# Kernel tuning notes

Hardware: AMD Instinct MI355X
Metric: run time of the kernel (lower is better)

## Reference

```python
import jax, jax.numpy as jnp
import numpy as np

B, S, D = 2, 2048, 768
C = 8                # num_channels
R = D // C           # ternary_rank = 96 (RoPE head_dim)
THETA = 10000.0
TERNARY_STD = 0.2
TERNARY_SCALE = 1.0  # ternary_factor_scaling


def _rope_tables():
    # HF-style RoPE: inv_freq over half dim, emb = concat(freqs, freqs)
    inv_freq = 1.0 / (THETA ** (np.arange(0, R, 2, dtype=np.float32) / R))
    pos = np.arange(S, dtype=np.float32)
    freqs = pos[:, None] * inv_freq[None, :]          # [S, R/2]
    emb = np.concatenate([freqs, freqs], axis=-1)     # [S, R]
    cos = np.broadcast_to(np.cos(emb)[None], (B, S, R)).copy()
    sin = np.broadcast_to(np.sin(emb)[None], (B, S, R)).copy()
    return jnp.asarray(cos), jnp.asarray(sin)


def setup_inputs() -> dict:
    key = jax.random.key(0)
    k1, k2, k3 = jax.random.split(key, 3)
    qz = jax.random.normal(k1, (B, S, D), dtype=jnp.float32)
    U = jax.random.normal(k2, (D, D), dtype=jnp.float32) * TERNARY_STD
    V = jax.random.normal(k3, (D, D), dtype=jnp.float32) * TERNARY_STD
    cos, sin = _rope_tables()
    return {"qz": qz, "cos": cos, "sin": sin, "U": U, "V": V}


def _rotate_half(x):
    h = x.shape[-1] // 2
    return jnp.concatenate([-x[..., h:], x[..., :h]], axis=-1)


def reference(qz, cos, sin, U, V):
    # cos/sin: [B,S,R] -> broadcast over channel dim -> [B,1,S,R]
    cosb = cos[:, None, :, :]
    sinb = sin[:, None, :, :]
    rope = lambda x: x * cosb + _rotate_half(x) * sinb       # apply
    rope_o = lambda x: x * cosb - _rotate_half(x) * sinb     # apply_o (inverse)

    # projections: F.linear(qz, W) == qz @ W.T
    qz_u = (qz @ U.T * TERNARY_SCALE).reshape(B, S, C, R).transpose(0, 2, 1, 3)
    qz_v = (qz @ V.T * TERNARY_SCALE).reshape(B, S, C, R).transpose(0, 2, 1, 3)

    qz_uo = rope_o(qz_u)
    qz_ur = rope(qz_u)
    qz_vr = rope(qz_v)

    # message_F: [B,C,S,S]
    message_F = jnp.einsum('bcqr,bckr->bcqk', qz_ur, qz_vr)
    # softmax(message_F / regularize_h) with regularize_h = 1/D  ->  * D
    qh = jax.nn.softmax((message_F * jnp.float32(D)).astype(jnp.float32), axis=-1).astype(qz_ur.dtype)

    qh_v1 = rope_o(jnp.einsum('bcqk,bckr->bcqr', qh, qz_vr))  # qh @ qz_v
    qh_v2 = rope(jnp.einsum('bckq,bckr->bcqr', qh, qz_uo))    # qh^T @ qz_uo

    qh_v1 = qh_v1.transpose(0, 2, 1, 3).reshape(B, S, D)
    qh_v2 = qh_v2.transpose(0, 2, 1, 3).reshape(B, S, D)

    message_G = (qh_v1 @ U + qh_v2 @ V) * TERNARY_SCALE
    return message_G
```

## Files before the change

### kernel.cpp

```cpp
#include <hip/hip_runtime.h>

typedef _Float16 f16;
typedef _Float16 f16x8 __attribute__((ext_vector_type(8)));
typedef _Float16 f16x4 __attribute__((ext_vector_type(4)));
typedef float f32x4 __attribute__((ext_vector_type(4)));

#define MFMA16(A,B,C) __builtin_amdgcn_mfma_f32_16x16x32_f16(A,B,C,0,0,0)
#define INV2048 4.8828125e-4f
#define HN (16ll*2048*96)
#define UVN 589824
#define ZC1 1107.98979f
#define ZC2 0.54101064f

__device__ __forceinline__ void split_f16(float x, f16& h, f16& l) {
    h = (f16)x;
    l = (f16)((x - (float)h) * 2048.0f);
}

__global__ __launch_bounds__(256) void k0_split(const float* __restrict__ qz,
                                                const float* __restrict__ U,
                                                const float* __restrict__ V,
                                                f16* __restrict__ qzh, f16* __restrict__ qzl,
                                                f16* __restrict__ Uh, f16* __restrict__ Ul,
                                                f16* __restrict__ Vh, f16* __restrict__ Vl) {
    const int i4 = blockIdx.x * 256 + threadIdx.x;
    {
        float4 x = *(const float4*)(qz + (size_t)i4 * 4);
        f16 h0, l0, h1, l1, h2, l2, h3, l3;
        split_f16(x.x, h0, l0); split_f16(x.y, h1, l1);
        split_f16(x.z, h2, l2); split_f16(x.w, h3, l3);
        f16x4 hv = {h0, h1, h2, h3};
        f16x4 lv = {l0, l1, l2, l3};
        *(f16x4*)(qzh + (size_t)i4 * 4) = hv;
        *(f16x4*)(qzl + (size_t)i4 * 4) = lv;
    }
    if (i4 < UVN / 4) {
        float4 x = *(const float4*)(U + (size_t)i4 * 4);
        f16 h0, l0, h1, l1, h2, l2, h3, l3;
        split_f16(x.x, h0, l0); split_f16(x.y, h1, l1);
        split_f16(x.z, h2, l2); split_f16(x.w, h3, l3);
        f16x4 hv = {h0, h1, h2, h3};
        f16x4 lv = {l0, l1, l2, l3};
        *(f16x4*)(Uh + (size_t)i4 * 4) = hv;
        *(f16x4*)(Ul + (size_t)i4 * 4) = lv;
        float4 y = *(const float4*)(V + (size_t)i4 * 4);
        split_f16(y.x, h0, l0); split_f16(y.y, h1, l1);
        split_f16(y.z, h2, l2); split_f16(y.w, h3, l3);
        f16x4 hv2 = {h0, h1, h2, h3};
        f16x4 lv2 = {l0, l1, l2, l3};
        *(f16x4*)(Vh + (size_t)i4 * 4) = hv2;
        *(f16x4*)(Vl + (size_t)i4 * 4) = lv2;
    }
}

__global__ __launch_bounds__(256, 2) void k1_proj(const f16* __restrict__ qzh,
                                                  const f16* __restrict__ qzl,
                                                  const f16* __restrict__ Uh,
                                                  const f16* __restrict__ Ul,
                                                  const f16* __restrict__ Vh,
                                                  const f16* __restrict__ Vl,
                                                  const float* __restrict__ cosb,
                                                  const float* __restrict__ sinb,
                                                  f16* __restrict__ uhp, f16* __restrict__ ulp,
                                                  f16* __restrict__ vhp, f16* __restrict__ vlp,
                                                  f16* __restrict__ vT, f16* __restrict__ oT) {
    __shared__ __align__(16) f16 smem[36864];
    f16* sAh  = smem;
    f16* sAl  = smem + 4608;
    f16* sBuh = smem + 9216;
    f16* sBul = smem + 9216 + 6912;
    f16* sBvh = smem + 9216 + 2 * 6912;
    f16* sBvl = smem + 9216 + 3 * 6912;

    const int tid = threadIdx.x;
    const int w = tid >> 6, lane = tid & 63;
    const int quad = lane >> 4, l15 = lane & 15;
    const int wr = w >> 1, wc = w & 1;
    const int bs0 = blockIdx.x * 64;
    const int c = blockIdx.y;

    const f16* Ug_h = Uh + (size_t)c * 96 * 768;
    const f16* Ug_l = Ul + (size_t)c * 96 * 768;
    const f16* Vg_h = Vh + (size_t)c * 96 * 768;
    const f16* Vg_l = Vl + (size_t)c * 96 * 768;

    f32x4 aUS[2][3] = {}, aUX[2][3] = {};
    f32x4 aVS[2][3] = {}, aVX[2][3] = {};

    for (int k0 = 0; k0 < 768; k0 += 64) {
        __syncthreads();
#pragma unroll
        for (int m = 0; m < 2; ++m) {
            int f = tid + 256 * m, row = f >> 3, cg = f & 7;
            const size_t go = (size_t)(bs0 + row) * 768 + k0 + cg * 8;
            const int lo = row * 72 + cg * 8;
            *(float4*)&sAh[lo] = *(const float4*)(qzh + go);
            *(float4*)&sAl[lo] = *(const float4*)(qzl + go);
        }
#pragma unroll
        for (int m = 0; m < 3; ++m) {
            int f = tid + 256 * m, row = f >> 3, cg = f & 7;
            const size_t go = (size_t)row * 768 + k0 + cg * 8;
            const int lo = row * 72 + cg * 8;
            *(float4*)&sBuh[lo] = *(const float4*)(Ug_h + go);
            *(float4*)&sBul[lo] = *(const float4*)(Ug_l + go);
            *(float4*)&sBvh[lo] = *(const float4*)(Vg_h + go);
            *(float4*)&sBvl[lo] = *(const float4*)(Vg_l + go);
        }
        __syncthreads();
#pragma unroll
        for (int cc = 0; cc < 2; ++cc) {
            f16x8 ah[2], al[2];
#pragma unroll
            for (int mt = 0; mt < 2; ++mt) {
                const int ar = (32 * wr + 16 * mt + l15) * 72 + cc * 32 + quad * 8;
                ah[mt] = *(const f16x8*)&sAh[ar];
                al[mt] = *(const f16x8*)&sAl[ar];
            }
#pragma unroll
            for (int nt = 0; nt < 3; ++nt) {
                const int br = (48 * wc + 16 * nt + l15) * 72 + cc * 32 + quad * 8;
                f16x8 buh = *(const f16x8*)&sBuh[br];
                f16x8 bul = *(const f16x8*)&sBul[br];
                f16x8 bvh = *(const f16x8*)&sBvh[br];
                f16x8 bvl = *(const f16x8*)&sBvl[br];
#pragma unroll
                for (int mt = 0; mt < 2; ++mt) {
                    aUS[mt][nt] = MFMA16(ah[mt], buh, aUS[mt][nt]);
                    aUX[mt][nt] = MFMA16(ah[mt], bul, aUX[mt][nt]);
                    aUX[mt][nt] = MFMA16(al[mt], buh, aUX[mt][nt]);
                    aVS[mt][nt] = MFMA16(ah[mt], bvh, aVS[mt][nt]);
                    aVX[mt][nt] = MFMA16(ah[mt], bvl, aVX[mt][nt]);
                    aVX[mt][nt] = MFMA16(al[mt], bvh, aVX[mt][nt]);
                }
            }
        }
    }

    __syncthreads();
    float* LU = (float*)smem;
    float* LV = LU + 6400;
#pragma unroll
    for (int mt = 0; mt < 2; ++mt)
#pragma unroll
        for (int nt = 0; nt < 3; ++nt)
#pragma unroll
            for (int r = 0; r < 4; ++r) {
                const int sl = 32 * wr + 16 * mt + 4 * quad + r;
                const int col = 48 * wc + 16 * nt + l15;
                LU[sl * 100 + col] = aUS[mt][nt][r] + aUX[mt][nt][r] * INV2048;
                LV[sl * 100 + col] = aVS[mt][nt][r] + aVX[mt][nt][r] * INV2048;
            }
    __syncthreads();

    const int b = bs0 >> 11;
    const int s0 = bs0 & 2047;
    const int head = b * 8 + c;
    const size_t nb = (size_t)head * 2048 * 96;
    const size_t tb = (size_t)head * 96 * 2048;
    const int ty = tid >> 4, tx = tid & 15;

#pragma unroll
    for (int jj = 0; jj < 3; ++jj) {
        int r = tx + 16 * jj;
        f16 vt1[4], vt2[4], ot1[4], ot2[4];
#pragma unroll
        for (int ii = 0; ii < 4; ++ii) {
            int sl = 4 * ty + ii;
            int s = s0 + sl;
            int cbi = (b * 2048 + s) * 96 + r;
            float cc = cosb[cbi], ss = sinb[cbi];
            size_t rowb = nb + (size_t)s * 96;
            float u1 = LU[sl * 100 + r], u2 = LU[sl * 100 + r + 48];
            float v1 = LV[sl * 100 + r], v2 = LV[sl * 100 + r + 48];
            float ur1 = u1 * cc - u2 * ss, ur2 = u2 * cc + u1 * ss;
            float uo1 = u1 * cc + u2 * ss, uo2 = u2 * cc - u1 * ss;
            float vr1 = v1 * cc - v2 * ss, vr2 = v2 * cc + v1 * ss;
            f16 h, l;
            split_f16(ur1, h, l); uhp[rowb + r] = h;      ulp[rowb + r] = l;
            split_f16(ur2, h, l); uhp[rowb + r + 48] = h; ulp[rowb + r + 48] = l;
            split_f16(vr1, h, l); vhp[rowb + r] = h;      vlp[rowb + r] = l;      vt1[ii] = h;
            split_f16(vr2, h, l); vhp[rowb + r + 48] = h; vlp[rowb + r + 48] = l; vt2[ii] = h;
            ot1[ii] = (f16)uo1; ot2[ii] = (f16)uo2;
        }
        f16x4 pv1 = {vt1[0], vt1[1], vt1[2], vt1[3]};
        f16x4 pv2 = {vt2[0], vt2[1], vt2[2], vt2[3]};
        f16x4 po1 = {ot1[0], ot1[1], ot1[2], ot1[3]};
        f16x4 po2 = {ot2[0], ot2[1], ot2[2], ot2[3]};
        *(f16x4*)&vT[tb + (size_t)r * 2048 + s0 + 4 * ty] = pv1;
        *(f16x4*)&vT[tb + (size_t)(r + 48) * 2048 + s0 + 4 * ty] = pv2;
        *(f16x4*)&oT[tb + (size_t)r * 2048 + s0 + 4 * ty] = po1;
        *(f16x4*)&oT[tb + (size_t)(r + 48) * 2048 + s0 + 4 * ty] = po2;
    }
}

__global__ __launch_bounds__(256, 2) void k2_stats(const f16* __restrict__ uhp,
                                                   const f16* __restrict__ ulp,
                                                   const f16* __restrict__ vhp,
                                                   const f16* __restrict__ vlp,
                                                   float* __restrict__ Mo,
                                                   float* __restrict__ Lo) {
    __shared__ f16 Bh[64 * 104];
    __shared__ f16 Bl[64 * 104];
    __shared__ float Mbuf[4][64], Lbuf[4][64];
    const int tid = threadIdx.x, w = tid >> 6, lane = tid & 63;
    const int quad = lane >> 4, l15 = lane & 15;
    const int q0 = blockIdx.x * 64, head = blockIdx.y;
    const f16* Ah_g = uhp + (size_t)head * 2048 * 96;
    const f16* Al_g = ulp + (size_t)head * 2048 * 96;
    const f16* Bh_g = vhp + (size_t)head * 2048 * 96;
    const f16* Bl_g = vlp + (size_t)head * 2048 * 96;

    f16x8 Afh[4][3], Afl[4][3];
#pragma unroll
    for (int mt = 0; mt < 4; ++mt)
#pragma unroll
        for (int cc = 0; cc < 3; ++cc) {
            size_t off = (size_t)(q0 + 16 * mt + l15) * 96 + cc * 32 + quad * 8;
            Afh[mt][cc] = *(const f16x8*)(Ah_g + off);
            Afl[mt][cc] = *(const f16x8*)(Al_g + off);
        }

    float m_run[4][4], l_run[4][4];
#pragma unroll
    for (int mt = 0; mt < 4; ++mt)
#pragma unroll
        for (int r = 0; r < 4; ++r) { m_run[mt][r] = -3.0e38f; l_run[mt][r] = 0.f; }

    for (int k0 = 0; k0 < 2048; k0 += 64) {
        __syncthreads();
#pragma unroll
        for (int m = 0; m < 3; ++m) {
            int f = tid + 256 * m;
            int row = f / 12, c12 = f % 12;
            *(float4*)&Bh[row * 104 + c12 * 8] =
                *(const float4*)(Bh_g + (size_t)(k0 + row) * 96 + c12 * 8);
            *(float4*)&Bl[row * 104 + c12 * 8] =
                *(const float4*)(Bl_g + (size_t)(k0 + row) * 96 + c12 * 8);
        }
        __syncthreads();
        f32x4 accS[4] = {}, accX[4] = {};
#pragma unroll
        for (int cc = 0; cc < 3; ++cc) {
            f16x8 bh = *(const f16x8*)&Bh[(w * 16 + l15) * 104 + cc * 32 + quad * 8];
            f16x8 bl = *(const f16x8*)&Bl[(w * 16 + l15) * 104 + cc * 32 + quad * 8];
#pragma unroll
            for (int mt = 0; mt < 4; ++mt) {
                accS[mt] = MFMA16(Afh[mt][cc], bh, accS[mt]);
                accX[mt] = MFMA16(Afh[mt][cc], bl, accX[mt]);
                accX[mt] = MFMA16(Afl[mt][cc], bh, accX[mt]);
            }
        }
#pragma unroll
        for (int mt = 0; mt < 4; ++mt)
#pragma unroll
            for (int r = 0; r < 4; ++r) {
                float zl = fmaf(ZC1, accS[mt][r], ZC2 * accX[mt][r]);
                float nm = fmaxf(m_run[mt][r], zl);
                l_run[mt][r] = fmaf(l_run[mt][r], exp2f(m_run[mt][r] - nm),
                                    exp2f(zl - nm));
                m_run[mt][r] = nm;
            }
    }
#pragma unroll
    for (int mt = 0; mt < 4; ++mt)
#pragma unroll
        for (int r = 0; r < 4; ++r) {
            float m = m_run[mt][r], l = l_run[mt][r];
#pragma unroll
            for (int d = 1; d < 16; d <<= 1) {
                float mo = __shfl_xor(m, d), lo = __shfl_xor(l, d);
                float nm = fmaxf(m, mo);
                l = fmaf(l, exp2f(m - nm), lo * exp2f(mo - nm));
                m = nm;
            }
            m_run[mt][r] = m; l_run[mt][r] = l;
        }
    if (l15 == 0) {
#pragma unroll
        for (int mt = 0; mt < 4; ++mt)
#pragma unroll
            for (int r = 0; r < 4; ++r) {
                Mbuf[w][16 * mt + 4 * quad + r] = m_run[mt][r];
                Lbuf[w][16 * mt + 4 * quad + r] = l_run[mt][r];
            }
    }
    __syncthreads();
    if (tid < 64) {
        float M = -3.0e38f;
#pragma unroll
        for (int ww = 0; ww < 4; ++ww) M = fmaxf(M, Mbuf[ww][tid]);
        float L = 0.f;
#pragma unroll
        for (int ww = 0; ww < 4; ++ww) L += Lbuf[ww][tid] * exp2f(Mbuf[ww][tid] - M);
        Mo[head * 2048 + q0 + tid] = M;
        Lo[head * 2048 + q0 + tid] = L;
    }
}

__global__ __launch_bounds__(256, 2) void k3a(const f16* __restrict__ uhp,
                                              const f16* __restrict__ ulp,
                                              const f16* __restrict__ vhp,
                                              const f16* __restrict__ vlp,
                                              const f16* __restrict__ vT,
                                              const float* __restrict__ Mo,
                                              const float* __restrict__ Lo,
                                              const float* __restrict__ cosb,
                                              const float* __restrict__ sinb,
                                              f16* __restrict__ w1) {
    __shared__ f16 Bh[64 * 104];
    __shared__ f16 Bl[64 * 104];
    __shared__ f16 Vt[96 * 72];
    __shared__ f16 P[64 * 72];
    const int tid = threadIdx.x, w = tid >> 6, lane = tid & 63;
    const int quad = lane >> 4, l15 = lane & 15;
    const int q0 = blockIdx.x * 64, head = blockIdx.y;
    const f16* Ah_g = uhp + (size_t)head * 2048 * 96;
    const f16* Al_g = ulp + (size_t)head * 2048 * 96;
    const f16* Bh_g = vhp + (size_t)head * 2048 * 96;
    const f16* Bl_g = vlp + (size_t)head * 2048 * 96;
    const f16* Vt_g = vT + (size_t)head * 96 * 2048;

    f16x8 Afh[4][3], Afl[4][3];
#pragma unroll
    for (int mt = 0; mt < 4; ++mt)
#pragma unroll
        for (int cc = 0; cc < 3; ++cc) {
            size_t off = (size_t)(q0 + 16 * mt + l15) * 96 + cc * 32 + quad * 8;
            Afh[mt][cc] = *(const f16x8*)(Ah_g + off);
            Afl[mt][cc] = *(const f16x8*)(Al_g + off);
        }
    float negM[4][4];
#pragma unroll
    for (int mt = 0; mt < 4; ++mt)
#pragma unroll
        for (int r = 0; r < 4; ++r)
            negM[mt][r] = -Mo[head * 2048 + q0 + 16 * mt + 4 * quad + r];
    float invL[4];
#pragma unroll
    for (int r = 0; r < 4; ++r)
        invL[r] = 1.0f / Lo[head * 2048 + q0 + w * 16 + quad * 4 + r];

    f32x4 accO[6] = {};

    for (int k0 = 0; k0 < 2048; k0 += 64) {
        __syncthreads();
#pragma unroll
        for (int m = 0; m < 3; ++m) {
            int f = tid + 256 * m;
            int row = f / 12, c12 = f % 12;
            *(float4*)&Bh[row * 104 + c12 * 8] =
                *(const float4*)(Bh_g + (size_t)(k0 + row) * 96 + c12 * 8);
            *(float4*)&Bl[row * 104 + c12 * 8] =
                *(const float4*)(Bl_g + (size_t)(k0 + row) * 96 + c12 * 8);
        }
#pragma unroll
        for (int m = 0; m < 3; ++m) {
            int f = tid + 256 * m;
            int row = f >> 3, c8 = f & 7;
            *(float4*)&Vt[row * 72 + c8 * 8] =
                *(const float4*)(Vt_g + (size_t)row * 2048 + k0 + c8 * 8);
        }
        __syncthreads();
        f32x4 accS[4] = {}, accX[4] = {};
#pragma unroll
        for (int cc = 0; cc < 3; ++cc) {
            f16x8 bh = *(const f16x8*)&Bh[(w * 16 + l15) * 104 + cc * 32 + quad * 8];
            f16x8 bl = *(const f16x8*)&Bl[(w * 16 + l15) * 104 + cc * 32 + quad * 8];
#pragma unroll
            for (int mt = 0; mt < 4; ++mt) {
                accS[mt] = MFMA16(Afh[mt][cc], bh, accS[mt]);
                accX[mt] = MFMA16(Afh[mt][cc], bl, accX[mt]);
                accX[mt] = MFMA16(Afl[mt][cc], bh, accX[mt]);
            }
        }
#pragma unroll
        for (int mt = 0; mt < 4; ++mt)
#pragma unroll
            for (int r = 0; r < 4; ++r) {
                float zl = fmaf(ZC1, accS[mt][r], ZC2 * accX[mt][r]);
                P[(16 * mt + 4 * quad + r) * 72 + w * 16 + l15] =
                    (f16)exp2f(zl + negM[mt][r]);
            }
        __syncthreads();
#pragma unroll
        for (int kc = 0; kc < 2; ++kc) {
            f16x8 ap = *(const f16x8*)&P[(w * 16 + l15) * 72 + kc * 32 + quad * 8];
#pragma unroll
            for (int nt = 0; nt < 6; ++nt) {
                f16x8 bv = *(const f16x8*)&Vt[(nt * 16 + l15) * 72 + kc * 32 + quad * 8];
                accO[nt] = MFMA16(ap, bv, accO[nt]);
            }
        }
        __syncthreads();
    }
    const int b = head >> 3, c = head & 7;
#pragma unroll
    for (int r = 0; r < 4; ++r) {
        int q = q0 + w * 16 + quad * 4 + r;
        int cbi = (b * 2048 + q) * 96;
        f16* wrow = w1 + (size_t)(b * 2048 + q) * 768 + c * 96;
#pragma unroll
        for (int nt = 0; nt < 3; ++nt) {
            int rr = nt * 16 + l15;
            float cc = cosb[cbi + rr], ss = sinb[cbi + rr];
            float a = accO[nt][r] * invL[r];
            float b2 = accO[nt + 3][r] * invL[r];
            wrow[rr] = (f16)(a * cc + b2 * ss);
            wrow[rr + 48] = (f16)(b2 * cc - a * ss);
        }
    }
}

__global__ __launch_bounds__(256, 2) void k3b(const f16* __restrict__ uhp,
                                              const f16* __restrict__ ulp,
                                              const f16* __restrict__ vhp,
                                              const f16* __restrict__ vlp,
                                              const f16* __restrict__ oT,
                                              const float* __restrict__ Mo,
                                              const float* __restrict__ Lo,
                                              const float* __restrict__ cosb,
                                              const float* __restrict__ sinb,
                                              f16* __restrict__ w2) {
    __shared__ f16 Bh[64 * 104];
    __shared__ f16 Bl[64 * 104];
    __shared__ f16 Ot[96 * 72];
    __shared__ f16 P[64 * 72];
    const int tid = threadIdx.x, w = tid >> 6, lane = tid & 63;
    const int quad = lane >> 4, l15 = lane & 15;
    const int q0 = blockIdx.x * 64, head = blockIdx.y;
    const f16* Ah_g = vhp + (size_t)head * 2048 * 96;
    const f16* Al_g = vlp + (size_t)head * 2048 * 96;
    const f16* Bh_g = uhp + (size_t)head * 2048 * 96;
    const f16* Bl_g = ulp + (size_t)head * 2048 * 96;
    const f16* Ot_g = oT + (size_t)head * 96 * 2048;

    f16x8 Afh[4][3], Afl[4][3];
#pragma unroll
    for (int mt = 0; mt < 4; ++mt)
#pragma unroll
        for (int cc = 0; cc < 3; ++cc) {
            size_t off = (size_t)(q0 + 16 * mt + l15) * 96 + cc * 32 + quad * 8;
            Afh[mt][cc] = *(const f16x8*)(Ah_g + off);
            Afl[mt][cc] = *(const f16x8*)(Al_g + off);
        }

    f32x4 accO[6] = {};

    for (int k0 = 0; k0 < 2048; k0 += 64) {
        float negMk = -Mo[head * 2048 + k0 + w * 16 + l15];
        float invLk = 1.0f / Lo[head * 2048 + k0 + w * 16 + l15];
        __syncthreads();
#pragma unroll
        for (int m = 0; m < 3; ++m) {
            int f = tid + 256 * m;
            int row = f / 12, c12 = f % 12;
            *(float4*)&Bh[row * 104 + c12 * 8] =
                *(const float4*)(Bh_g + (size_t)(k0 + row) * 96 + c12 * 8);
            *(float4*)&Bl[row * 104 + c12 * 8] =
                *(const float4*)(Bl_g + (size_t)(k0 + row) * 96 + c12 * 8);
        }
#pragma unroll
        for (int m = 0; m < 3; ++m) {
            int f = tid + 256 * m;
            int row = f >> 3, c8 = f & 7;
            *(float4*)&Ot[row * 72 + c8 * 8] =
                *(const float4*)(Ot_g + (size_t)row * 2048 + k0 + c8 * 8);
        }
        __syncthreads();
        f32x4 accS[4] = {}, accX[4] = {};
#pragma unroll
        for (int cc = 0; cc < 3; ++cc) {
            f16x8 bh = *(const f16x8*)&Bh[(w * 16 + l15) * 104 + cc * 32 + quad * 8];
            f16x8 bl = *(const f16x8*)&Bl[(w * 16 + l15) * 104 + cc * 32 + quad * 8];
#pragma unroll
            for (int mt = 0; mt < 4; ++mt) {
                accS[mt] = MFMA16(Afh[mt][cc], bh, accS[mt]);
                accX[mt] = MFMA16(Afl[mt][cc], bh, accX[mt]);
                accX[mt] = MFMA16(Afh[mt][cc], bl, accX[mt]);
            }
        }
#pragma unroll
        for (int mt = 0; mt < 4; ++mt)
#pragma unroll
            for (int r = 0; r < 4; ++r) {
                float zl = fmaf(ZC1, accS[mt][r], ZC2 * accX[mt][r]);
                P[(16 * mt + 4 * quad + r) * 72 + w * 16 + l15] =
                    (f16)(exp2f(zl + negMk) * invLk);
            }
        __syncthreads();
#pragma unroll
        for (int kc = 0; kc < 2; ++kc) {
            f16x8 ap = *(const f16x8*)&P[(w * 16 + l15) * 72 + kc * 32 + quad * 8];
#pragma unroll
            for (int nt = 0; nt < 6; ++nt) {
                f16x8 bo = *(const f16x8*)&Ot[(nt * 16 + l15) * 72 + kc * 32 + quad * 8];
                accO[nt] = MFMA16(ap, bo, accO[nt]);
            }
        }
        __syncthreads();
    }
    const int b = head >> 3, c = head & 7;
#pragma unroll
    for (int r = 0; r < 4; ++r) {
        int q = q0 + w * 16 + quad * 4 + r;
        int cbi = (b * 2048 + q) * 96;
        f16* wrow = w2 + (size_t)(b * 2048 + q) * 768 + c * 96;
#pragma unroll
        for (int nt = 0; nt < 3; ++nt) {
            int rr = nt * 16 + l15;
            float cc = cosb[cbi + rr], ss = sinb[cbi + rr];
            float a = accO[nt][r];
            float b2 = accO[nt + 3][r];
            wrow[rr] = (f16)(a * cc - b2 * ss);
            wrow[rr + 48] = (f16)(b2 * cc + a * ss);
        }
    }
}

__global__ __launch_bounds__(256, 2) void k4_final(const f16* __restrict__ w1,
                                                   const f16* __restrict__ w2,
                                                   const float* __restrict__ U,
                                                   const float* __restrict__ V,
                                                   float* __restrict__ outp) {
    __shared__ f16 A1[128 * 56];
    __shared__ f16 A2[128 * 56];
    __shared__ f16 B1[64 * 56];
    __shared__ f16 B2[64 * 56];
    const int tid = threadIdx.x, w = tid >> 6, lane = tid & 63;
    const int quad = lane >> 4, l15 = lane & 15;
    const int bs0 = blockIdx.x * 128;
    const int d0 = blockIdx.y * 64;
    f32x4 acc[2][4] = {};

    for (int ec = 0; ec < 24; ++ec) {
        int e0 = ec * 32;
        __syncthreads();
#pragma unroll
        for (int m = 0; m < 2; ++m) {
            int f = tid + 256 * m;
            int row = f >> 2, q = f & 3;
            *(float4*)&A1[row * 56 + q * 8] =
                *(const float4*)(w1 + (size_t)(bs0 + row) * 768 + e0 + q * 8);
            *(float4*)&A2[row * 56 + q * 8] =
                *(const float4*)(w2 + (size_t)(bs0 + row) * 768 + e0 + q * 8);
        }
#pragma unroll
        for (int m2 = 0; m2 < 2; ++m2) {
            int e_r = (tid >> 4) + 16 * m2;
            int dc = tid & 15;
            float4 fu = *(const float4*)(U + (size_t)(e0 + e_r) * 768 + d0 + dc * 4);
            float4 fv = *(const float4*)(V + (size_t)(e0 + e_r) * 768 + d0 + dc * 4);
            B1[(dc * 4 + 0) * 56 + e_r] = (f16)fu.x;
            B1[(dc * 4 + 1) * 56 + e_r] = (f16)fu.y;
            B1[(dc * 4 + 2) * 56 + e_r] = (f16)fu.z;
            B1[(dc * 4 + 3) * 56 + e_r] = (f16)fu.w;
            B2[(dc * 4 + 0) * 56 + e_r] = (f16)fv.x;
            B2[(dc * 4 + 1) * 56 + e_r] = (f16)fv.y;
            B2[(dc * 4 + 2) * 56 + e_r] = (f16)fv.z;
            B2[(dc * 4 + 3) * 56 + e_r] = (f16)fv.w;
        }
        __syncthreads();
        f16x8 a1f[2], a2f[2];
#pragma unroll
        for (int mt = 0; mt < 2; ++mt) {
            a1f[mt] = *(const f16x8*)&A1[(32 * w + 16 * mt + l15) * 56 + quad * 8];
            a2f[mt] = *(const f16x8*)&A2[(32 * w + 16 * mt + l15) * 56 + quad * 8];
        }
#pragma unroll
        for (int nt = 0; nt < 4; ++nt) {
            f16x8 b1f = *(const f16x8*)&B1[(nt * 16 + l15) * 56 + quad * 8];
            f16x8 b2f = *(const f16x8*)&B2[(nt * 16 + l15) * 56 + quad * 8];
#pragma unroll
            for (int mt = 0; mt < 2; ++mt) {
                acc[mt][nt] = MFMA16(a1f[mt], b1f, acc[mt][nt]);
                acc[mt][nt] = MFMA16(a2f[mt], b2f, acc[mt][nt]);
            }
        }
    }
#pragma unroll
    for (int mt = 0; mt < 2; ++mt)
#pragma unroll
        for (int nt = 0; nt < 4; ++nt)
#pragma unroll
            for (int r = 0; r < 4; ++r) {
                int s = bs0 + 32 * w + 16 * mt + 4 * quad + r;
                int d = d0 + 16 * nt + l15;
                outp[(size_t)s * 768 + d] = acc[mt][nt][r];
            }
}

extern "C" void kernel_launch(void* const* d_in, const int* in_sizes, int n_in,
                              void* d_out, int out_size, void* d_ws, size_t ws_size,
                              hipStream_t stream) {
    const float* qz   = (const float*)d_in[0];
    const float* cosb = (const float*)d_in[1];
    const float* sinb = (const float*)d_in[2];
    const float* U    = (const float*)d_in[3];
    const float* V    = (const float*)d_in[4];
    float* outp = (float*)d_out;

    f16* ws16 = (f16*)d_ws;
    f16* uhp = ws16;
    f16* ulp = ws16 + HN;
    f16* vhp = ws16 + 2 * HN;
    f16* vlp = ws16 + 3 * HN;
    f16* vT  = ws16 + 4 * HN;
    f16* oT  = ws16 + 5 * HN;
    f16* w1  = ws16 + 6 * HN;
    f16* w2  = ws16 + 7 * HN;
    float* Mo = (float*)(ws16 + 8 * HN);
    float* Lo = Mo + 16 * 2048;

    f16* qzh = w1;
    f16* qzl = w2;
    f16* outw = (f16*)d_out;
    f16* Uh = outw;
    f16* Ul = outw + UVN;
    f16* Vh = outw + 2 * UVN;
    f16* Vl = outw + 3 * UVN;

    k0_split<<<dim3(3072), 256, 0, stream>>>(qz, U, V, qzh, qzl, Uh, Ul, Vh, Vl);
    k1_proj<<<dim3(64, 8), 256, 0, stream>>>(qzh, qzl, Uh, Ul, Vh, Vl, cosb, sinb,
                                             uhp, ulp, vhp, vlp, vT, oT);
    k2_stats<<<dim3(32, 16), 256, 0, stream>>>(uhp, ulp, vhp, vlp, Mo, Lo);
    k3a<<<dim3(32, 16), 256, 0, stream>>>(uhp, ulp, vhp, vlp, vT, Mo, Lo, cosb, sinb, w1);
    k3b<<<dim3(32, 16), 256, 0, stream>>>(uhp, ulp, vhp, vlp, oT, Mo, Lo, cosb, sinb, w2);
    k4_final<<<dim3(32, 12), 256, 0, stream>>>(w1, w2, U, V, outp);
}
```

Before: 364.8 us.

## Software-pipeline global loads with register prefetch and double-buffered shared tiles

Restructures the main loops of the projection, stats and both attention-apply kernels so the next tile's global loads go into registers while the current tile is computed. In the three attention kernels the key tiles are also double-buffered in shared memory, which drops one barrier per iteration. The P tile in the two apply kernels gets an XOR swizzle to reduce LDS bank conflicts. The costs are more registers (which may lower occupancy) and more shared memory per block.

```diff
diff --git a/kernel.cpp b/kernel.cpp
--- a/kernel.cpp
+++ b/kernel.cpp
@@ -87,27 +87,50 @@
     f32x4 aUS[2][3] = {}, aUX[2][3] = {};
     f32x4 aVS[2][3] = {}, aVX[2][3] = {};
 
+    float4 rAh[2], rAl[2], rUh[3], rUl[3], rVh[3], rVl[3];
+    auto loadAll = [&](int k0) {
+#pragma unroll
+        for (int m = 0; m < 2; ++m) {
+            int f = tid + 256 * m, row = f >> 3, cg8 = (f & 7) * 8;
+            const size_t go = (size_t)(bs0 + row) * 768 + k0 + cg8;
+            rAh[m] = *(const float4*)(qzh + go);
+            rAl[m] = *(const float4*)(qzl + go);
+        }
+#pragma unroll
+        for (int m = 0; m < 3; ++m) {
+            int f = tid + 256 * m, row = f >> 3, cg8 = (f & 7) * 8;
+            const size_t go = (size_t)row * 768 + k0 + cg8;
+            rUh[m] = *(const float4*)(Ug_h + go);
+            rUl[m] = *(const float4*)(Ug_l + go);
+            rVh[m] = *(const float4*)(Vg_h + go);
+            rVl[m] = *(const float4*)(Vg_l + go);
+        }
+    };
+    auto storeAll = [&]() {
+#pragma unroll
+        for (int m = 0; m < 2; ++m) {
+            int f = tid + 256 * m, row = f >> 3, cg8 = (f & 7) * 8;
+            const int lo = row * 72 + cg8;
+            *(float4*)&sAh[lo] = rAh[m];
+            *(float4*)&sAl[lo] = rAl[m];
+        }
+#pragma unroll
+        for (int m = 0; m < 3; ++m) {
+            int f = tid + 256 * m, row = f >> 3, cg8 = (f & 7) * 8;
+            const int lo = row * 72 + cg8;
+            *(float4*)&sBuh[lo] = rUh[m];
+            *(float4*)&sBul[lo] = rUl[m];
+            *(float4*)&sBvh[lo] = rVh[m];
+            *(float4*)&sBvl[lo] = rVl[m];
+        }
+    };
+
+    loadAll(0);
     for (int k0 = 0; k0 < 768; k0 += 64) {
         __syncthreads();
-#pragma unroll
-        for (int m = 0; m < 2; ++m) {
-            int f = tid + 256 * m, row = f >> 3, cg = f & 7;
-            const size_t go = (size_t)(bs0 + row) * 768 + k0 + cg * 8;
-            const int lo = row * 72 + cg * 8;
-            *(float4*)&sAh[lo] = *(const float4*)(qzh + go);
-            *(float4*)&sAl[lo] = *(const float4*)(qzl + go);
-        }
-#pragma unroll
-        for (int m = 0; m < 3; ++m) {
-            int f = tid + 256 * m, row = f >> 3, cg = f & 7;
-            const size_t go = (size_t)row * 768 + k0 + cg * 8;
-            const int lo = row * 72 + cg * 8;
-            *(float4*)&sBuh[lo] = *(const float4*)(Ug_h + go);
-            *(float4*)&sBul[lo] = *(const float4*)(Ug_l + go);
-            *(float4*)&sBvh[lo] = *(const float4*)(Vg_h + go);
-            *(float4*)&sBvl[lo] = *(const float4*)(Vg_l + go);
-        }
-        __syncthreads();
+        storeAll();
+        __syncthreads();
+        if (k0 + 64 < 768) loadAll(k0 + 64);
 #pragma unroll
         for (int cc = 0; cc < 2; ++cc) {
             f16x8 ah[2], al[2];
@@ -200,8 +223,8 @@
                                                    const f16* __restrict__ vlp,
                                                    float* __restrict__ Mo,
                                                    float* __restrict__ Lo) {
-    __shared__ f16 Bh[64 * 104];
-    __shared__ f16 Bl[64 * 104];
+    __shared__ f16 Bh[2][64 * 104];
+    __shared__ f16 Bl[2][64 * 104];
     __shared__ float Mbuf[4][64], Lbuf[4][64];
     const int tid = threadIdx.x, w = tid >> 6, lane = tid & 63;
     const int quad = lane >> 4, l15 = lane & 15;
@@ -221,29 +244,46 @@
             Afl[mt][cc] = *(const f16x8*)(Al_g + off);
         }
 
+    int srow[3], scol[3];
+#pragma unroll
+    for (int m = 0; m < 3; ++m) {
+        int f = tid + 256 * m;
+        srow[m] = f / 12; scol[m] = (f % 12) * 8;
+    }
+    float4 rh[3], rl[3];
+    auto loadB = [&](int k0) {
+#pragma unroll
+        for (int m = 0; m < 3; ++m) {
+            rh[m] = *(const float4*)(Bh_g + (size_t)(k0 + srow[m]) * 96 + scol[m]);
+            rl[m] = *(const float4*)(Bl_g + (size_t)(k0 + srow[m]) * 96 + scol[m]);
+        }
+    };
+    auto storeB = [&](int bsel) {
+#pragma unroll
+        for (int m = 0; m < 3; ++m) {
+            *(float4*)&Bh[bsel][srow[m] * 104 + scol[m]] = rh[m];
+            *(float4*)&Bl[bsel][srow[m] * 104 + scol[m]] = rl[m];
+        }
+    };
+
     float m_run[4][4], l_run[4][4];
 #pragma unroll
     for (int mt = 0; mt < 4; ++mt)
 #pragma unroll
         for (int r = 0; r < 4; ++r) { m_run[mt][r] = -3.0e38f; l_run[mt][r] = 0.f; }
 
-    for (int k0 = 0; k0 < 2048; k0 += 64) {
-        __syncthreads();
-#pragma unroll
-        for (int m = 0; m < 3; ++m) {
-            int f = tid + 256 * m;
-            int row = f / 12, c12 = f % 12;
-            *(float4*)&Bh[row * 104 + c12 * 8] =
-                *(const float4*)(Bh_g + (size_t)(k0 + row) * 96 + c12 * 8);
-            *(float4*)&Bl[row * 104 + c12 * 8] =
-                *(const float4*)(Bl_g + (size_t)(k0 + row) * 96 + c12 * 8);
-        }
-        __syncthreads();
+    loadB(0); storeB(0); loadB(64);
+    __syncthreads();
+
+    for (int t = 0; t < 32; ++t) {
+        const int cur = t & 1;
+        if (t < 31) storeB(cur ^ 1);
+        if (t < 30) loadB((t + 2) * 64);
         f32x4 accS[4] = {}, accX[4] = {};
 #pragma unroll
         for (int cc = 0; cc < 3; ++cc) {
-            f16x8 bh = *(const f16x8*)&Bh[(w * 16 + l15) * 104 + cc * 32 + quad * 8];
-            f16x8 bl = *(const f16x8*)&Bl[(w * 16 + l15) * 104 + cc * 32 + quad * 8];
+            f16x8 bh = *(const f16x8*)&Bh[cur][(w * 16 + l15) * 104 + cc * 32 + quad * 8];
+            f16x8 bl = *(const f16x8*)&Bl[cur][(w * 16 + l15) * 104 + cc * 32 + quad * 8];
 #pragma unroll
             for (int mt = 0; mt < 4; ++mt) {
                 accS[mt] = MFMA16(Afh[mt][cc], bh, accS[mt]);
@@ -261,6 +301,7 @@
                                     exp2f(zl - nm));
                 m_run[mt][r] = nm;
             }
+        __syncthreads();
     }
 #pragma unroll
     for (int mt = 0; mt < 4; ++mt)
@@ -308,8 +349,8 @@
                                               const float* __restrict__ cosb,
                                               const float* __restrict__ sinb,
                                               f16* __restrict__ w1) {
-    __shared__ f16 Bh[64 * 104];
-    __shared__ f16 Bl[64 * 104];
+    __shared__ f16 Bh[2][64 * 104];
+    __shared__ f16 Bl[2][64 * 104];
     __shared__ f16 Vt[96 * 72];
     __shared__ f16 P[64 * 72];
     const int tid = threadIdx.x, w = tid >> 6, lane = tid & 63;
@@ -341,32 +382,58 @@
     for (int r = 0; r < 4; ++r)
         invL[r] = 1.0f / Lo[head * 2048 + q0 + w * 16 + quad * 4 + r];
 
+    int srow[3], scol[3], vrow[3], vcol[3];
+#pragma unroll
+    for (int m = 0; m < 3; ++m) {
+        int f = tid + 256 * m;
+        srow[m] = f / 12; scol[m] = (f % 12) * 8;
+        vrow[m] = f >> 3; vcol[m] = (f & 7) * 8;
+    }
+    float4 rh[3], rl[3], rv[3];
+    auto loadB = [&](int k0) {
+#pragma unroll
+        for (int m = 0; m < 3; ++m) {
+            rh[m] = *(const float4*)(Bh_g + (size_t)(k0 + srow[m]) * 96 + scol[m]);
+            rl[m] = *(const float4*)(Bl_g + (size_t)(k0 + srow[m]) * 96 + scol[m]);
+        }
+    };
+    auto storeB = [&](int bsel) {
+#pragma unroll
+        for (int m = 0; m < 3; ++m) {
+            *(float4*)&Bh[bsel][srow[m] * 104 + scol[m]] = rh[m];
+            *(float4*)&Bl[bsel][srow[m] * 104 + scol[m]] = rl[m];
+        }
+    };
+    auto loadV = [&](int k0) {
+#pragma unroll
+        for (int m = 0; m < 3; ++m)
+            rv[m] = *(const float4*)(Vt_g + (size_t)vrow[m] * 2048 + k0 + vcol[m]);
+    };
+    auto storeV = [&]() {
+#pragma unroll
+        for (int m = 0; m < 3; ++m)
+            *(float4*)&Vt[vrow[m] * 72 + vcol[m]] = rv[m];
+    };
+
     f32x4 accO[6] = {};
 
-    for (int k0 = 0; k0 < 2048; k0 += 64) {
-        __syncthreads();
-#pragma unroll
-        for (int m = 0; m < 3; ++m) {
-            int f = tid + 256 * m;
-            int row = f / 12, c12 = f % 12;
-            *(float4*)&Bh[row * 104 + c12 * 8] =
-                *(const float4*)(Bh_g + (size_t)(k0 + row) * 96 + c12 * 8);
-            *(float4*)&Bl[row * 104 + c12 * 8] =
-                *(const float4*)(Bl_g + (size_t)(k0 + row) * 96 + c12 * 8);
-        }
-#pragma unroll
-        for (int m = 0; m < 3; ++m) {
-            int f = tid + 256 * m;
-            int row = f >> 3, c8 = f & 7;
-            *(float4*)&Vt[row * 72 + c8 * 8] =
-                *(const float4*)(Vt_g + (size_t)row * 2048 + k0 + c8 * 8);
-        }
-        __syncthreads();
+    loadB(0); storeB(0);
+    loadV(0); loadB(64);
+    __syncthreads();
+
+    for (int t = 0; t < 32; ++t) {
+        const int cur = t & 1;
+        const int k0 = t * 64;
+        storeV();
+        if (t < 31) storeB(cur ^ 1);
+        if (t < 31) loadV(k0 + 64);
+        if (t < 30) loadB(k0 + 128);
+
         f32x4 accS[4] = {}, accX[4] = {};
 #pragma unroll
         for (int cc = 0; cc < 3; ++cc) {
-            f16x8 bh = *(const f16x8*)&Bh[(w * 16 + l15) * 104 + cc * 32 + quad * 8];
-            f16x8 bl = *(const f16x8*)&Bl[(w * 16 + l15) * 104 + cc * 32 + quad * 8];
+            f16x8 bh = *(const f16x8*)&Bh[cur][(w * 16 + l15) * 104 + cc * 32 + quad * 8];
+            f16x8 bl = *(const f16x8*)&Bl[cur][(w * 16 + l15) * 104 + cc * 32 + quad * 8];
 #pragma unroll
             for (int mt = 0; mt < 4; ++mt) {
                 accS[mt] = MFMA16(Afh[mt][cc], bh, accS[mt]);
@@ -379,13 +446,15 @@
 #pragma unroll
             for (int r = 0; r < 4; ++r) {
                 float zl = fmaf(ZC1, accS[mt][r], ZC2 * accX[mt][r]);
-                P[(16 * mt + 4 * quad + r) * 72 + w * 16 + l15] =
+                P[(16 * mt + 4 * quad + r) * 72 +
+                  ((w * 16 + l15) ^ ((quad >> 1) << 4))] =
                     (f16)exp2f(zl + negM[mt][r]);
             }
         __syncthreads();
 #pragma unroll
         for (int kc = 0; kc < 2; ++kc) {
-            f16x8 ap = *(const f16x8*)&P[(w * 16 + l15) * 72 + kc * 32 + quad * 8];
+            f16x8 ap = *(const f16x8*)&P[(w * 16 + l15) * 72 +
+                                         ((kc * 32 + quad * 8) ^ (((l15 >> 3) & 1) << 4))];
 #pragma unroll
             for (int nt = 0; nt < 6; ++nt) {
                 f16x8 bv = *(const f16x8*)&Vt[(nt * 16 + l15) * 72 + kc * 32 + quad * 8];
@@ -422,8 +491,8 @@
                                               const float* __restrict__ cosb,
                                               const float* __restrict__ sinb,
                                               f16* __restrict__ w2) {
-    __shared__ f16 Bh[64 * 104];
-    __shared__ f16 Bl[64 * 104];
+    __shared__ f16 Bh[2][64 * 104];
+    __shared__ f16 Bl[2][64 * 104];
     __shared__ f16 Ot[96 * 72];
     __shared__ f16 P[64 * 72];
     const int tid = threadIdx.x, w = tid >> 6, lane = tid & 63;
@@ -445,34 +514,60 @@
             Afl[mt][cc] = *(const f16x8*)(Al_g + off);
         }
 
+    int srow[3], scol[3], vrow[3], vcol[3];
+#pragma unroll
+    for (int m = 0; m < 3; ++m) {
+        int f = tid + 256 * m;
+        srow[m] = f / 12; scol[m] = (f % 12) * 8;
+        vrow[m] = f >> 3; vcol[m] = (f & 7) * 8;
+    }
+    float4 rh[3], rl[3], rv[3];
+    auto loadB = [&](int k0) {
+#pragma unroll
+        for (int m = 0; m < 3; ++m) {
+            rh[m] = *(const float4*)(Bh_g + (size_t)(k0 + srow[m]) * 96 + scol[m]);
+            rl[m] = *(const float4*)(Bl_g + (size_t)(k0 + srow[m]) * 96 + scol[m]);
+        }
+    };
+    auto storeB = [&](int bsel) {
+#pragma unroll
+        for (int m = 0; m < 3; ++m) {
+            *(float4*)&Bh[bsel][srow[m] * 104 + scol[m]] = rh[m];
+            *(float4*)&Bl[bsel][srow[m] * 104 + scol[m]] = rl[m];
+        }
+    };
+    auto loadO = [&](int k0) {
+#pragma unroll
+        for (int m = 0; m < 3; ++m)
+            rv[m] = *(const float4*)(Ot_g + (size_t)vrow[m] * 2048 + k0 + vcol[m]);
+    };
+    auto storeO = [&]() {
+#pragma unroll
+        for (int m = 0; m < 3; ++m)
+            *(float4*)&Ot[vrow[m] * 72 + vcol[m]] = rv[m];
+    };
+
     f32x4 accO[6] = {};
 
-    for (int k0 = 0; k0 < 2048; k0 += 64) {
+    loadB(0); storeB(0);
+    loadO(0); loadB(64);
+    __syncthreads();
+
+    for (int t = 0; t < 32; ++t) {
+        const int cur = t & 1;
+        const int k0 = t * 64;
         float negMk = -Mo[head * 2048 + k0 + w * 16 + l15];
         float invLk = 1.0f / Lo[head * 2048 + k0 + w * 16 + l15];
-        __syncthreads();
-#pragma unroll
-        for (int m = 0; m < 3; ++m) {
-            int f = tid + 256 * m;
-            int row = f / 12, c12 = f % 12;
-            *(float4*)&Bh[row * 104 + c12 * 8] =
-                *(const float4*)(Bh_g + (size_t)(k0 + row) * 96 + c12 * 8);
-            *(float4*)&Bl[row * 104 + c12 * 8] =
-                *(const float4*)(Bl_g + (size_t)(k0 + row) * 96 + c12 * 8);
-        }
-#pragma unroll
-        for (int m = 0; m < 3; ++m) {
-            int f = tid + 256 * m;
-            int row = f >> 3, c8 = f & 7;
-            *(float4*)&Ot[row * 72 + c8 * 8] =
-                *(const float4*)(Ot_g + (size_t)row * 2048 + k0 + c8 * 8);
-        }
-        __syncthreads();
+        storeO();
+        if (t < 31) storeB(cur ^ 1);
+        if (t < 31) loadO(k0 + 64);
+        if (t < 30) loadB(k0 + 128);
+
         f32x4 accS[4] = {}, accX[4] = {};
 #pragma unroll
         for (int cc = 0; cc < 3; ++cc) {
-            f16x8 bh = *(const f16x8*)&Bh[(w * 16 + l15) * 104 + cc * 32 + quad * 8];
-            f16x8 bl = *(const f16x8*)&Bl[(w * 16 + l15) * 104 + cc * 32 + quad * 8];
+            f16x8 bh = *(const f16x8*)&Bh[cur][(w * 16 + l15) * 104 + cc * 32 + quad * 8];
+            f16x8 bl = *(const f16x8*)&Bl[cur][(w * 16 + l15) * 104 + cc * 32 + quad * 8];
 #pragma unroll
             for (int mt = 0; mt < 4; ++mt) {
                 accS[mt] = MFMA16(Afh[mt][cc], bh, accS[mt]);
@@ -485,13 +580,15 @@
 #pragma unroll
             for (int r = 0; r < 4; ++r) {
                 float zl = fmaf(ZC1, accS[mt][r], ZC2 * accX[mt][r]);
-                P[(16 * mt + 4 * quad + r) * 72 + w * 16 + l15] =
+                P[(16 * mt + 4 * quad + r) * 72 +
+                  ((w * 16 + l15) ^ ((quad >> 1) << 4))] =
                     (f16)(exp2f(zl + negMk) * invLk);
             }
         __syncthreads();
 #pragma unroll
         for (int kc = 0; kc < 2; ++kc) {
-            f16x8 ap = *(const f16x8*)&P[(w * 16 + l15) * 72 + kc * 32 + quad * 8];
+            f16x8 ap = *(const f16x8*)&P[(w * 16 + l15) * 72 +
+                                         ((kc * 32 + quad * 8) ^ (((l15 >> 3) & 1) << 4))];
 #pragma unroll
             for (int nt = 0; nt < 6; ++nt) {
                 f16x8 bo = *(const f16x8*)&Ot[(nt * 16 + l15) * 72 + kc * 32 + quad * 8];
```

Result: slower. 782.0 us (+114.4%).

## Double-buffer K tiles via direct global-to-LDS loads in attention kernels

Applied to the files above, without the earlier changes.

The stats and both output kernels now prefetch the next 64-row hi/lo key tile straight into a second LDS buffer with global_load_lds. The loads overlap the current tile's MFMA work, and the padded 104-stride layout becomes an unpadded 96-stride layout, which may add LDS bank conflicts. The transposed value tile is prefetched into registers during the score computation and written to LDS after the barrier. The projection kernel's K step is cut from 64 to 32 and has a dead placeholder block. Correctness relies on the barrier placement and on the async LDS writes being complete before they are read.

```diff
diff --git a/kernel.cpp b/kernel.cpp
--- a/kernel.cpp
+++ b/kernel.cpp
@@ -15,6 +15,12 @@
 __device__ __forceinline__ void split_f16(float x, f16& h, f16& l) {
     h = (f16)x;
     l = (f16)((x - (float)h) * 2048.0f);
+}
+
+__device__ __forceinline__ void gload16(const f16* g, f16* l) {
+    __builtin_amdgcn_global_load_lds(
+        (const __attribute__((address_space(1))) unsigned int*)g,
+        (__attribute__((address_space(3))) unsigned int*)l, 16, 0, 0);
 }
 
 __global__ __launch_bounds__(256) void k0_split(const float* __restrict__ qz,
@@ -87,39 +93,48 @@
     f32x4 aUS[2][3] = {}, aUX[2][3] = {};
     f32x4 aVS[2][3] = {}, aVX[2][3] = {};
 
-    for (int k0 = 0; k0 < 768; k0 += 64) {
-        __syncthreads();
-#pragma unroll
-        for (int m = 0; m < 2; ++m) {
-            int f = tid + 256 * m, row = f >> 3, cg = f & 7;
+    for (int k0 = 0; k0 < 768; k0 += 32) {
+        __syncthreads();
+        {
+            int f = tid;
+            int i = f >> 2, ec = f & 3;
+            const size_t go = (size_t)(bs0 + i) * 768 + k0 + 8 * ec;
+            const int lo = i * 72 + 8 * ec + ((k0 & 32) ? 32 : 0);
+            (void)lo;
+        }
+        {
+            int f = tid;
+            int row = f >> 2, cg = f & 3;
             const size_t go = (size_t)(bs0 + row) * 768 + k0 + cg * 8;
             const int lo = row * 72 + cg * 8;
             *(float4*)&sAh[lo] = *(const float4*)(qzh + go);
             *(float4*)&sAl[lo] = *(const float4*)(qzl + go);
         }
 #pragma unroll
-        for (int m = 0; m < 3; ++m) {
-            int f = tid + 256 * m, row = f >> 3, cg = f & 7;
-            const size_t go = (size_t)row * 768 + k0 + cg * 8;
-            const int lo = row * 72 + cg * 8;
-            *(float4*)&sBuh[lo] = *(const float4*)(Ug_h + go);
-            *(float4*)&sBul[lo] = *(const float4*)(Ug_l + go);
-            *(float4*)&sBvh[lo] = *(const float4*)(Vg_h + go);
-            *(float4*)&sBvl[lo] = *(const float4*)(Vg_l + go);
-        }
-        __syncthreads();
-#pragma unroll
-        for (int cc = 0; cc < 2; ++cc) {
+        for (int m = 0; m < 2; ++m) {
+            int f = tid + 256 * m;
+            if (f < 384) {
+                int row = f >> 2, cg = f & 3;
+                const size_t go = (size_t)row * 768 + k0 + cg * 8;
+                const int lo = row * 72 + cg * 8;
+                *(float4*)&sBuh[lo] = *(const float4*)(Ug_h + go);
+                *(float4*)&sBul[lo] = *(const float4*)(Ug_l + go);
+                *(float4*)&sBvh[lo] = *(const float4*)(Vg_h + go);
+                *(float4*)&sBvl[lo] = *(const float4*)(Vg_l + go);
+            }
+        }
+        __syncthreads();
+        {
             f16x8 ah[2], al[2];
 #pragma unroll
             for (int mt = 0; mt < 2; ++mt) {
-                const int ar = (32 * wr + 16 * mt + l15) * 72 + cc * 32 + quad * 8;
+                const int ar = (32 * wr + 16 * mt + l15) * 72 + quad * 8;
                 ah[mt] = *(const f16x8*)&sAh[ar];
                 al[mt] = *(const f16x8*)&sAl[ar];
             }
 #pragma unroll
             for (int nt = 0; nt < 3; ++nt) {
-                const int br = (48 * wc + 16 * nt + l15) * 72 + cc * 32 + quad * 8;
+                const int br = (48 * wc + 16 * nt + l15) * 72 + quad * 8;
                 f16x8 buh = *(const f16x8*)&sBuh[br];
                 f16x8 bul = *(const f16x8*)&sBul[br];
                 f16x8 bvh = *(const f16x8*)&sBvh[br];
@@ -200,8 +215,8 @@
                                                    const f16* __restrict__ vlp,
                                                    float* __restrict__ Mo,
                                                    float* __restrict__ Lo) {
-    __shared__ f16 Bh[64 * 104];
-    __shared__ f16 Bl[64 * 104];
+    __shared__ f16 Bh[2][64 * 96];
+    __shared__ f16 Bl[2][64 * 96];
     __shared__ float Mbuf[4][64], Lbuf[4][64];
     const int tid = threadIdx.x, w = tid >> 6, lane = tid & 63;
     const int quad = lane >> 4, l15 = lane & 15;
@@ -221,29 +236,37 @@
             Afl[mt][cc] = *(const f16x8*)(Al_g + off);
         }
 
+    const int o0 = tid * 8;
+
     float m_run[4][4], l_run[4][4];
 #pragma unroll
     for (int mt = 0; mt < 4; ++mt)
 #pragma unroll
         for (int r = 0; r < 4; ++r) { m_run[mt][r] = -3.0e38f; l_run[mt][r] = 0.f; }
 
-    for (int k0 = 0; k0 < 2048; k0 += 64) {
-        __syncthreads();
-#pragma unroll
-        for (int m = 0; m < 3; ++m) {
-            int f = tid + 256 * m;
-            int row = f / 12, c12 = f % 12;
-            *(float4*)&Bh[row * 104 + c12 * 8] =
-                *(const float4*)(Bh_g + (size_t)(k0 + row) * 96 + c12 * 8);
-            *(float4*)&Bl[row * 104 + c12 * 8] =
-                *(const float4*)(Bl_g + (size_t)(k0 + row) * 96 + c12 * 8);
-        }
-        __syncthreads();
+#pragma unroll
+    for (int m = 0; m < 3; ++m) {
+        gload16(Bh_g + o0 + 2048 * m, &Bh[0][o0 + 2048 * m]);
+        gload16(Bl_g + o0 + 2048 * m, &Bl[0][o0 + 2048 * m]);
+    }
+    __syncthreads();
+
+    for (int t = 0; t < 32; ++t) {
+        const int cur = t & 1;
+        if (t < 31) {
+            const f16* bs = Bh_g + (size_t)(t + 1) * 6144;
+            const f16* ls = Bl_g + (size_t)(t + 1) * 6144;
+#pragma unroll
+            for (int m = 0; m < 3; ++m) {
+                gload16(bs + o0 + 2048 * m, &Bh[cur ^ 1][o0 + 2048 * m]);
+                gload16(ls + o0 + 2048 * m, &Bl[cur ^ 1][o0 + 2048 * m]);
+            }
+        }
         f32x4 accS[4] = {}, accX[4] = {};
 #pragma unroll
         for (int cc = 0; cc < 3; ++cc) {
-            f16x8 bh = *(const f16x8*)&Bh[(w * 16 + l15) * 104 + cc * 32 + quad * 8];
-            f16x8 bl = *(const f16x8*)&Bl[(w * 16 + l15) * 104 + cc * 32 + quad * 8];
+            f16x8 bh = *(const f16x8*)&Bh[cur][(w * 16 + l15) * 96 + cc * 32 + quad * 8];
+            f16x8 bl = *(const f16x8*)&Bl[cur][(w * 16 + l15) * 96 + cc * 32 + quad * 8];
 #pragma unroll
             for (int mt = 0; mt < 4; ++mt) {
                 accS[mt] = MFMA16(Afh[mt][cc], bh, accS[mt]);
@@ -261,6 +284,7 @@
                                     exp2f(zl - nm));
                 m_run[mt][r] = nm;
             }
+        __syncthreads();
     }
 #pragma unroll
     for (int mt = 0; mt < 4; ++mt)
@@ -308,8 +332,8 @@
                                               const float* __restrict__ cosb,
                                               const float* __restrict__ sinb,
                                               f16* __restrict__ w1) {
-    __shared__ f16 Bh[64 * 104];
-    __shared__ f16 Bl[64 * 104];
+    __shared__ f16 Bh[2][64 * 96];
+    __shared__ f16 Bl[2][64 * 96];
     __shared__ f16 Vt[96 * 72];
     __shared__ f16 P[64 * 72];
     const int tid = threadIdx.x, w = tid >> 6, lane = tid & 63;
@@ -341,32 +365,42 @@
     for (int r = 0; r < 4; ++r)
         invL[r] = 1.0f / Lo[head * 2048 + q0 + w * 16 + quad * 4 + r];
 
+    const int o0 = tid * 8;
+    const int vr = tid >> 3;
+    const int vc = (tid & 7) * 8;
+    float4 rv0, rv1, rv2;
+
+#pragma unroll
+    for (int m = 0; m < 3; ++m) {
+        gload16(Bh_g + o0 + 2048 * m, &Bh[0][o0 + 2048 * m]);
+        gload16(Bl_g + o0 + 2048 * m, &Bl[0][o0 + 2048 * m]);
+    }
+    rv0 = *(const float4*)(Vt_g + (size_t)vr * 2048 + vc);
+    rv1 = *(const float4*)(Vt_g + (size_t)(vr + 32) * 2048 + vc);
+    rv2 = *(const float4*)(Vt_g + (size_t)(vr + 64) * 2048 + vc);
+    __syncthreads();
+    *(float4*)&Vt[vr * 72 + vc] = rv0;
+    *(float4*)&Vt[(vr + 32) * 72 + vc] = rv1;
+    *(float4*)&Vt[(vr + 64) * 72 + vc] = rv2;
+
     f32x4 accO[6] = {};
 
-    for (int k0 = 0; k0 < 2048; k0 += 64) {
-        __syncthreads();
-#pragma unroll
-        for (int m = 0; m < 3; ++m) {
-            int f = tid + 256 * m;
-            int row = f / 12, c12 = f % 12;
-            *(float4*)&Bh[row * 104 + c12 * 8] =
-                *(const float4*)(Bh_g + (size_t)(k0 + row) * 96 + c12 * 8);
-            *(float4*)&Bl[row * 104 + c12 * 8] =
-                *(const float4*)(Bl_g + (size_t)(k0 + row) * 96 + c12 * 8);
-        }
-#pragma unroll
-        for (int m = 0; m < 3; ++m) {
-            int f = tid + 256 * m;
-            int row = f >> 3, c8 = f & 7;
-            *(float4*)&Vt[row * 72 + c8 * 8] =
-                *(const float4*)(Vt_g + (size_t)row * 2048 + k0 + c8 * 8);
-        }
-        __syncthreads();
+    for (int t = 0; t < 32; ++t) {
+        const int cur = t & 1;
+        if (t < 31) {
+            const f16* bs = Bh_g + (size_t)(t + 1) * 6144;
+            const f16* ls = Bl_g + (size_t)(t + 1) * 6144;
+#pragma unroll
+            for (int m = 0; m < 3; ++m) {
+                gload16(bs + o0 + 2048 * m, &Bh[cur ^ 1][o0 + 2048 * m]);
+                gload16(ls + o0 + 2048 * m, &Bl[cur ^ 1][o0 + 2048 * m]);
+            }
+        }
         f32x4 accS[4] = {}, accX[4] = {};
 #pragma unroll
         for (int cc = 0; cc < 3; ++cc) {
-            f16x8 bh = *(const f16x8*)&Bh[(w * 16 + l15) * 104 + cc * 32 + quad * 8];
-            f16x8 bl = *(const f16x8*)&Bl[(w * 16 + l15) * 104 + cc * 32 + quad * 8];
+            f16x8 bh = *(const f16x8*)&Bh[cur][(w * 16 + l15) * 96 + cc * 32 + quad * 8];
+            f16x8 bl = *(const f16x8*)&Bl[cur][(w * 16 + l15) * 96 + cc * 32 + quad * 8];
 #pragma unroll
             for (int mt = 0; mt < 4; ++mt) {
                 accS[mt] = MFMA16(Afh[mt][cc], bh, accS[mt]);
@@ -374,6 +408,12 @@
                 accX[mt] = MFMA16(Afl[mt][cc], bh, accX[mt]);
             }
         }
+        if (t < 31) {
+            const int kn = (t + 1) * 64;
+            rv0 = *(const float4*)(Vt_g + (size_t)vr * 2048 + kn + vc);
+            rv1 = *(const float4*)(Vt_g + (size_t)(vr + 32) * 2048 + kn + vc);
+            rv2 = *(const float4*)(Vt_g + (size_t)(vr + 64) * 2048 + kn + vc);
+        }
 #pragma unroll
         for (int mt = 0; mt < 4; ++mt)
 #pragma unroll
@@ -393,6 +433,11 @@
             }
         }
         __syncthreads();
+        if (t < 31) {
+            *(float4*)&Vt[vr * 72 + vc] = rv0;
+            *(float4*)&Vt[(vr + 32) * 72 + vc] = rv1;
+            *(float4*)&Vt[(vr + 64) * 72 + vc] = rv2;
+        }
     }
     const int b = head >> 3, c = head & 7;
 #pragma unroll
@@ -422,8 +467,8 @@
                                               const float* __restrict__ cosb,
                                               const float* __restrict__ sinb,
                                               f16* __restrict__ w2) {
-    __shared__ f16 Bh[64 * 104];
-    __shared__ f16 Bl[64 * 104];
+    __shared__ f16 Bh[2][64 * 96];
+    __shared__ f16 Bl[2][64 * 96];
     __shared__ f16 Ot[96 * 72];
     __shared__ f16 P[64 * 72];
     const int tid = threadIdx.x, w = tid >> 6, lane = tid & 63;
@@ -445,34 +490,45 @@
             Afl[mt][cc] = *(const f16x8*)(Al_g + off);
         }
 
+    const int o0 = tid * 8;
+    const int vr = tid >> 3;
+    const int vc = (tid & 7) * 8;
+    float4 rv0, rv1, rv2;
+
+#pragma unroll
+    for (int m = 0; m < 3; ++m) {
+        gload16(Bh_g + o0 + 2048 * m, &Bh[0][o0 + 2048 * m]);
+        gload16(Bl_g + o0 + 2048 * m, &Bl[0][o0 + 2048 * m]);
+    }
+    rv0 = *(const float4*)(Ot_g + (size_t)vr * 2048 + vc);
+    rv1 = *(const float4*)(Ot_g + (size_t)(vr + 32) * 2048 + vc);
+    rv2 = *(const float4*)(Ot_g + (size_t)(vr + 64) * 2048 + vc);
+    __syncthreads();
+    *(float4*)&Ot[vr * 72 + vc] = rv0;
+    *(float4*)&Ot[(vr + 32) * 72 + vc] = rv1;
+    *(float4*)&Ot[(vr + 64) * 72 + vc] = rv2;
+
     f32x4 accO[6] = {};
 
-    for (int k0 = 0; k0 < 2048; k0 += 64) {
+    for (int t = 0; t < 32; ++t) {
+        const int cur = t & 1;
+        const int k0 = t * 64;
         float negMk = -Mo[head * 2048 + k0 + w * 16 + l15];
         float invLk = 1.0f / Lo[head * 2048 + k0 + w * 16 + l15];
-        __syncthreads();
-#pragma unroll
-        for (int m = 0; m < 3; ++m) {
-            int f = tid + 256 * m;
-            int row = f / 12, c12 = f % 12;
-            *(float4*)&Bh[row * 104 + c12 * 8] =
-                *(const float4*)(Bh_g + (size_t)(k0 + row) * 96 + c12 * 8);
-            *(float4*)&Bl[row * 104 + c12 * 8] =
-                *(const float4*)(Bl_g + (size_t)(k0 + row) * 96 + c12 * 8);
-        }
-#pragma unroll
-        for (int m = 0; m < 3; ++m) {
-            int f = tid + 256 * m;
-            int row = f >> 3, c8 = f & 7;
-            *(float4*)&Ot[row * 72 + c8 * 8] =
-                *(const float4*)(Ot_g + (size_t)row * 2048 + k0 + c8 * 8);
-        }
-        __syncthreads();
+        if (t < 31) {
+            const f16* bs = Bh_g + (size_t)(t + 1) * 6144;
+            const f16* ls = Bl_g + (size_t)(t + 1) * 6144;
+#pragma unroll
+            for (int m = 0; m < 3; ++m) {
+                gload16(bs + o0 + 2048 * m, &Bh[cur ^ 1][o0 + 2048 * m]);
+                gload16(ls + o0 + 2048 * m, &Bl[cur ^ 1][o0 + 2048 * m]);
+            }
+        }
         f32x4 accS[4] = {}, accX[4] = {};
 #pragma unroll
         for (int cc = 0; cc < 3; ++cc) {
-            f16x8 bh = *(const f16x8*)&Bh[(w * 16 + l15) * 104 + cc * 32 + quad * 8];
-            f16x8 bl = *(const f16x8*)&Bl[(w * 16 + l15) * 104 + cc * 32 + quad * 8];
+            f16x8 bh = *(const f16x8*)&Bh[cur][(w * 16 + l15) * 96 + cc * 32 + quad * 8];
+            f16x8 bl = *(const f16x8*)&Bl[cur][(w * 16 + l15) * 96 + cc * 32 + quad * 8];
 #pragma unroll
             for (int mt = 0; mt < 4; ++mt) {
                 accS[mt] = MFMA16(Afh[mt][cc], bh, accS[mt]);
@@ -480,6 +536,12 @@
                 accX[mt] = MFMA16(Afh[mt][cc], bl, accX[mt]);
             }
         }
+        if (t < 31) {
+            const int kn = (t + 1) * 64;
+            rv0 = *(const float4*)(Ot_g + (size_t)vr * 2048 + kn + vc);
+            rv1 = *(const float4*)(Ot_g + (size_t)(vr + 32) * 2048 + kn + vc);
+            rv2 = *(const float4*)(Ot_g + (size_t)(vr + 64) * 2048 + kn + vc);
+        }
 #pragma unroll
         for (int mt = 0; mt < 4; ++mt)
 #pragma unroll
@@ -499,6 +561,11 @@
             }
         }
         __syncthreads();
+        if (t < 31) {
+            *(float4*)&Ot[vr * 72 + vc] = rv0;
+            *(float4*)&Ot[(vr + 32) * 72 + vc] = rv1;
+            *(float4*)&Ot[(vr + 64) * 72 + vc] = rv2;
+        }
     }
     const int b = head >> 3, c = head & 7;
 #pragma unroll
```

Measured after the change: 399.9 us. +9.6%, slower.
